# Performance work log

Measured on AMD Instinct MI355X. Metric: run time of the kernel, lower is better.

The kernel has to match this reference:

```python
import jax, jax.numpy as jnp
import numpy as np

B, S, D = 2, 4096, 768
H, DH = 12, 64
W = 256          # one-sided window (attention_window=512 // 2)
G = 8            # number of global tokens (first G positions)
NEG = -1e9


def setup_inputs() -> dict:
    key = jax.random.key(0)
    ks = jax.random.split(key, 8)
    hidden_states = jax.random.normal(ks[0], (B, S, D), dtype=jnp.float32)
    attention_mask = jnp.ones((B, S), dtype=jnp.float32)
    sc = 0.02
    Wq = jax.random.normal(ks[1], (D, D), dtype=jnp.float32) * sc
    Wk = jax.random.normal(ks[2], (D, D), dtype=jnp.float32) * sc
    Wv = jax.random.normal(ks[3], (D, D), dtype=jnp.float32) * sc
    Wqg = jax.random.normal(ks[4], (D, D), dtype=jnp.float32) * sc
    Wkg = jax.random.normal(ks[5], (D, D), dtype=jnp.float32) * sc
    Wvg = jax.random.normal(ks[6], (D, D), dtype=jnp.float32) * sc
    return {"hidden_states": hidden_states, "attention_mask": attention_mask,
            "Wq": Wq, "Wk": Wk, "Wv": Wv, "Wqg": Wqg, "Wkg": Wkg, "Wvg": Wvg}


def _heads(x):  # [B,S,D] -> [B,H,S,DH]
    return x.reshape(B, S, H, DH).transpose(0, 2, 1, 3)


def longformer_attn(hidden_states, attention_mask, Wq, Wk, Wv, Wqg, Wkg, Wvg):
    scale = 1.0 / jnp.sqrt(jnp.float32(DH))
    q = _heads(hidden_states @ Wq) * scale   # [B,H,S,DH]
    k = _heads(hidden_states @ Wk)
    v = _heads(hidden_states @ Wv)

    n = S // W                                # number of query chunks
    kp = jnp.pad(k, ((0, 0), (0, 0), (W, W), (0, 0)))
    vp = jnp.pad(v, ((0, 0), (0, 0), (W, W), (0, 0)))
    # window indices into padded seq: chunk i covers keys [i*W - W, i*W + 2W)
    idx = jnp.arange(n)[:, None] * W + jnp.arange(3 * W)[None, :]   # [n,3W]
    k_win = kp[:, :, idx]                     # [B,H,n,3W,DH]
    v_win = vp[:, :, idx]
    qc = q.reshape(B, H, n, W, DH)

    scores = jnp.einsum('bhnqd,bhnkd->bhnqk', qc, k_win)  # [B,H,n,W,3W]

    # masks: band (|key-query|<=W), valid key position, not a global key,
    # and key attention_mask
    rel = jnp.arange(3 * W)[None, :] - jnp.arange(W)[:, None]   # [W,3W] = k - q
    band = (rel >= 0) & (rel <= 2 * W)
    key_pos = idx - W                                           # [n,3W] real positions
    valid = (key_pos >= 0) & (key_pos < S) & (key_pos >= G)
    struct_mask = band[None, :, :] & valid[:, None, :]          # [n,W,3W]
    amp = jnp.pad(attention_mask, ((0, 0), (W, W)))
    am_win = amp[:, idx] > 0.5                                  # [B,n,3W]
    full_mask = struct_mask[None] & am_win[:, :, None, :]       # [B,n,W,3W]
    scores = jnp.where(full_mask[:, None], scores, NEG)

    # every query also attends to the G global keys (regular key projection)
    gk = k[:, :, :G]                                            # [B,H,G,DH]
    gscore = jnp.einsum('bhsd,bhgd->bhsg', q, gk).reshape(B, H, n, W, G)
    all_scores = jnp.concatenate([gscore, scores], axis=-1)     # [B,H,n,W,G+3W]
    probs = jax.nn.softmax(all_scores, axis=-1)

    gv = v[:, :, :G]
    out = (jnp.einsum('bhnqk,bhnkd->bhnqd', probs[..., G:], v_win)
           + jnp.einsum('bhnqg,bhgd->bhnqd', probs[..., :G], gv))
    out = out.reshape(B, H, S, DH)

    # global queries attend to ALL tokens with the *_global projections
    qg = _heads(hidden_states @ Wqg)[:, :, :G] * scale          # [B,H,G,DH]
    kg = _heads(hidden_states @ Wkg)
    vg = _heads(hidden_states @ Wvg)
    gs = jnp.einsum('bhgd,bhsd->bhgs', qg, kg)                  # [B,H,G,S]
    gs = jnp.where(attention_mask[:, None, None, :] > 0.5, gs, NEG)
    gp = jax.nn.softmax(gs, axis=-1)
    gout = jnp.einsum('bhgs,bhsd->bhgd', gp, vg)
    out = out.at[:, :, :G].set(gout)

    return out.transpose(0, 2, 1, 3).reshape(B, S, D)


def reference(hidden_states, attention_mask, Wq, Wk, Wv, Wqg, Wkg, Wvg):
    return longformer_attn(hidden_states, attention_mask, Wq, Wk, Wv, Wqg, Wkg, Wvg)
```

## Files before the change

kernel.cpp:

```cpp
#include <hip/hip_runtime.h>

#define B_ 2
#define S_ 4096
#define D_ 768
#define H_ 12
#define DH_ 64
#define W_ 256
#define G_ 8
#define NEG_ (-1e9f)
#define NC_ 64
#define CK_ 64
#define WQB 128
#define NT_ 11
#define NWIN (B_ * H_ * (S_ / WQB))

typedef __attribute__((ext_vector_type(4))) float f32x4;
typedef __attribute__((ext_vector_type(16))) float f32x16;
typedef __attribute__((ext_vector_type(8))) short s16x8;
typedef __attribute__((ext_vector_type(4))) short s16x4;
typedef unsigned short ushort_t;

__device__ __forceinline__ unsigned short f2bf(float f) {
    union { float f; unsigned u; } v; v.f = f;
    unsigned r = v.u + 0x7FFFu + ((v.u >> 16) & 1u);
    return (unsigned short)(r >> 16);
}
__device__ __forceinline__ float bf2f(unsigned short b) {
    union { unsigned u; float f; } v; v.u = ((unsigned)b) << 16;
    return v.f;
}
__device__ __forceinline__ unsigned cvtpk_bf16(float lo, float hi) {
    unsigned r;
    asm("v_cvt_pk_bf16_f32 %0, %1, %2" : "=v"(r) : "v"(lo), "v"(hi));
    return r;
}
__device__ __forceinline__ void gload16(const ushort_t* g, ushort_t* l) {
    __builtin_amdgcn_global_load_lds(
        (const __attribute__((address_space(1))) unsigned*)g,
        (__attribute__((address_space(3))) unsigned*)l, 16, 0, 0);
}
__device__ __forceinline__ float vmax16f(f32x16 v) {
    float a0 = fmaxf(v[0], v[1]), a1 = fmaxf(v[2], v[3]);
    float a2 = fmaxf(v[4], v[5]), a3 = fmaxf(v[6], v[7]);
    float a4 = fmaxf(v[8], v[9]), a5 = fmaxf(v[10], v[11]);
    float a6 = fmaxf(v[12], v[13]), a7 = fmaxf(v[14], v[15]);
    return fmaxf(fmaxf(fmaxf(a0, a1), fmaxf(a2, a3)),
                 fmaxf(fmaxf(a4, a5), fmaxf(a6, a7)));
}
__device__ __forceinline__ float vsum16f(f32x16 v) {
    float a0 = v[0] + v[1], a1 = v[2] + v[3];
    float a2 = v[4] + v[5], a3 = v[6] + v[7];
    float a4 = v[8] + v[9], a5 = v[10] + v[11];
    float a6 = v[12] + v[13], a7 = v[14] + v[15];
    return ((a0 + a1) + (a2 + a3)) + ((a4 + a5) + (a6 + a7));
}

__global__ __launch_bounds__(256) void fused_pre(const float* __restrict__ hs,
                                                 const float* __restrict__ W0,
                                                 const float* __restrict__ W1,
                                                 const float* __restrict__ W2,
                                                 const float* __restrict__ W3,
                                                 const float* __restrict__ W4,
                                                 const float* __restrict__ Wqg,
                                                 ushort_t* __restrict__ hs_bf,
                                                 ushort_t* __restrict__ wt,
                                                 float* __restrict__ qg) {
    __shared__ float smf[2 * D_];
    const int bid = blockIdx.x;
    const int t = threadIdx.x;

    if (bid < 3072) {
        const int i = bid * 256 + t;
        float4 a = *(const float4*)&hs[(size_t)i * 8];
        float4 c = *(const float4*)&hs[(size_t)i * 8 + 4];
        s16x8 o;
        o[0] = (short)f2bf(a.x); o[1] = (short)f2bf(a.y);
        o[2] = (short)f2bf(a.z); o[3] = (short)f2bf(a.w);
        o[4] = (short)f2bf(c.x); o[5] = (short)f2bf(c.y);
        o[6] = (short)f2bf(c.z); o[7] = (short)f2bf(c.w);
        *(s16x8*)&hs_bf[(size_t)i * 8] = o;
    } else if (bid < 5952) {
        const int bid2 = bid - 3072;
        const int w = bid2 / 576;
        const int rem = bid2 - w * 576;
        const int k0 = (rem / 24) * 32;
        const int n0 = (rem % 24) * 32;
        const float* Wsrc = (w == 0) ? W0 : (w == 1) ? W1 : (w == 2) ? W2 : (w == 3) ? W3 : W4;
        const float scl = (w == 0) ? 0.125f * 1.44269504f : 1.0f;
        const int r = t >> 3, c4 = (t & 7) * 4;
        float4 src = *(const float4*)&Wsrc[(size_t)(k0 + r) * D_ + n0 + c4];
        smf[r * 33 + c4 + 0] = src.x; smf[r * 33 + c4 + 1] = src.y;
        smf[r * 33 + c4 + 2] = src.z; smf[r * 33 + c4 + 3] = src.w;
        __syncthreads();
        s16x4 o;
        o[0] = (short)f2bf(smf[(c4 + 0) * 33 + r] * scl);
        o[1] = (short)f2bf(smf[(c4 + 1) * 33 + r] * scl);
        o[2] = (short)f2bf(smf[(c4 + 2) * 33 + r] * scl);
        o[3] = (short)f2bf(smf[(c4 + 3) * 33 + r] * scl);
        *(s16x4*)&wt[((size_t)(w * D_ + n0 + r)) * D_ + k0 + c4] = o;
    } else {
        const int bid3 = bid - 5952;
        const int rp = bid3 / 6;
        const int c0 = (bid3 - rp * 6) * 128;
        const int r = t >> 7, cl = t & 127;
        for (int i = t; i < 2 * D_; i += 256) {
            const int rr = i / D_, kk = i - rr * D_;
            const int row = rp * 2 + rr;
            const int b = row >> 3, g = row & 7;
            smf[rr * D_ + kk] = hs[((size_t)b * S_ + g) * D_ + kk];
        }
        __syncthreads();
        float a0 = 0.f, a1 = 0.f, a2 = 0.f, a3 = 0.f;
        const float* wp = &Wqg[c0 + cl];
        for (int kk = 0; kk < D_; kk += 4) {
            a0 += smf[r * D_ + kk + 0] * wp[(size_t)(kk + 0) * D_];
            a1 += smf[r * D_ + kk + 1] * wp[(size_t)(kk + 1) * D_];
            a2 += smf[r * D_ + kk + 2] * wp[(size_t)(kk + 2) * D_];
            a3 += smf[r * D_ + kk + 3] * wp[(size_t)(kk + 3) * D_];
        }
        const int row = rp * 2 + r;
        qg[(size_t)row * D_ + c0 + cl] = (a0 + a1 + a2 + a3) * 0.125f;
    }
}

__global__ __launch_bounds__(256, 2) void proj_mfma(const ushort_t* __restrict__ A,
                                                    const ushort_t* __restrict__ Bt,
                                                    ushort_t* __restrict__ oq,
                                                    ushort_t* __restrict__ ok,
                                                    ushort_t* __restrict__ ov,
                                                    ushort_t* __restrict__ okg,
                                                    ushort_t* __restrict__ ovg) {
    __shared__ char smem[34048];
    ushort_t* Al = (ushort_t*)smem;
    ushort_t* Bl = Al + 128 * 64;

    const int t = threadIdx.x;
    const int m0 = blockIdx.x * 128;
    const int n0 = blockIdx.y * 128;
    const int lane = t & 63;
    const int w = t >> 6;
    const int wm = (w >> 1) * 64, wn = (w & 1) * 64;
    const int ln = lane & 15, hi = lane >> 4;

    const int srow_in_call = lane >> 3;
    const int scol = ((lane & 7) ^ srow_in_call) * 8;

    f32x4 acc[4][4];
#pragma unroll
    for (int mi = 0; mi < 4; ++mi)
#pragma unroll
        for (int ni = 0; ni < 4; ++ni) acc[mi][ni] = (f32x4){0.f, 0.f, 0.f, 0.f};

    for (int k0 = 0; k0 < D_; k0 += 64) {
        __syncthreads();
#pragma unroll
        for (int j = 0; j < 4; ++j) {
            const int rbase = (w * 4 + j) * 8;
            const int row = rbase + srow_in_call;
            gload16(&A[(size_t)(m0 + row) * D_ + k0 + scol], &Al[rbase * 64]);
            gload16(&Bt[(size_t)(n0 + row) * D_ + k0 + scol], &Bl[rbase * 64]);
        }
        __syncthreads();

#pragma unroll
        for (int ks = 0; ks < 2; ++ks) {
            s16x8 af[4], bf[4];
#pragma unroll
            for (int i = 0; i < 4; ++i) {
                const int ar = wm + i * 16 + ln;
                const int br = wn + i * 16 + ln;
                const int slot = (4 * ks + hi) ^ (ln & 7);
                af[i] = *(const s16x8*)&Al[ar * 64 + slot * 8];
                bf[i] = *(const s16x8*)&Bl[br * 64 + slot * 8];
            }
#pragma unroll
            for (int mi = 0; mi < 4; ++mi)
#pragma unroll
                for (int ni = 0; ni < 4; ++ni)
                    acc[mi][ni] = __builtin_amdgcn_mfma_f32_16x16x32_bf16(af[mi], bf[ni], acc[mi][ni], 0, 0, 0);
        }
    }

    float* scr = (float*)smem;
    const int rl = t >> 2, cs = (t & 3) * 32;
    const int ng = n0 + cs;
    const int w_idx = ng / D_;
    const int cb = ng - w_idx * D_;
    const int hh = cb >> 6, dd = cb & 63;
    ushort_t* dst = (w_idx == 0) ? oq : (w_idx == 1) ? ok : (w_idx == 2) ? ov
                    : (w_idx == 3) ? okg : ovg;

#pragma unroll
    for (int r = 0; r < 2; ++r) {
        __syncthreads();
        if ((w >> 1) == r) {
#pragma unroll
            for (int mi = 0; mi < 4; ++mi)
#pragma unroll
                for (int ni = 0; ni < 4; ++ni)
#pragma unroll
                    for (int rr = 0; rr < 4; ++rr)
                        scr[(mi * 16 + hi * 4 + rr) * 132 + wn + ni * 16 + ln] = acc[mi][ni][rr];
        }
        __syncthreads();
        const int m = m0 + r * 64 + rl;
        const int bb = m >> 12, s = m & 4095;
        ushort_t* drow = dst + ((size_t)(bb * H_ + hh) * S_ + s) * DH_ + dd;
        const float* srcp = scr + rl * 132 + cs;
#pragma unroll
        for (int seg = 0; seg < 4; ++seg) {
            float4 lo = *(const float4*)&srcp[seg * 8];
            float4 hi4 = *(const float4*)&srcp[seg * 8 + 4];
            s16x8 o;
            o[0] = (short)f2bf(lo.x); o[1] = (short)f2bf(lo.y);
            o[2] = (short)f2bf(lo.z); o[3] = (short)f2bf(lo.w);
            o[4] = (short)f2bf(hi4.x); o[5] = (short)f2bf(hi4.y);
            o[6] = (short)f2bf(hi4.z); o[7] = (short)f2bf(hi4.w);
            *(s16x8*)&drow[seg * 8] = o;
        }
    }
}

__global__ __launch_bounds__(256, 2) void win_glob(const ushort_t* __restrict__ q,
                                                   const ushort_t* __restrict__ k,
                                                   const ushort_t* __restrict__ v,
                                                   const float* __restrict__ am,
                                                   float* __restrict__ out,
                                                   const float* __restrict__ qg,
                                                   const ushort_t* __restrict__ kg,
                                                   const ushort_t* __restrict__ vg,
                                                   float* __restrict__ pout,
                                                   float* __restrict__ pm,
                                                   float* __restrict__ pl) {
    __shared__ char smem[39424];
    const int bid = blockIdx.x;
    const int t = threadIdx.x;

    if (bid >= NWIN) {
        const int idx = bid - NWIN;
        const int c = idx & 63;
        const int hb = idx >> 6;
        const int h = hb % H_;
        const int b = hb / H_;
        const int bh = b * H_ + h;
        const size_t base = (size_t)bh * S_ * DH_;
        const int jg0 = c * CK_;

        float* qs = (float*)smem;
        float* kt = qs + G_ * DH_;
        float* vt = kt + CK_ * 69;
        float* ps = vt + CK_ * 68;

        for (int i = t; i < G_ * DH_; i += 256)
            qs[(i >> 6) * DH_ + (i & 63)] = qg[(size_t)(b * G_ + (i >> 6)) * D_ + h * DH_ + (i & 63)];
        {
            const int row = t >> 2, off = (t & 3) * 16;
            const ushort_t* kr = &kg[base + (size_t)(jg0 + row) * DH_ + off];
            const ushort_t* vr = &vg[base + (size_t)(jg0 + row) * DH_ + off];
            s16x8 ka = *(const s16x8*)kr;
            s16x8 kb2 = *(const s16x8*)(kr + 8);
            s16x8 va = *(const s16x8*)vr;
            s16x8 vb = *(const s16x8*)(vr + 8);
#pragma unroll
            for (int i = 0; i < 8; ++i) {
                kt[row * 69 + off + i] = bf2f((ushort_t)ka[i]);
                kt[row * 69 + off + 8 + i] = bf2f((ushort_t)kb2[i]);
                vt[row * 68 + off + i] = bf2f((ushort_t)va[i]);
                vt[row * 68 + off + 8 + i] = bf2f((ushort_t)vb[i]);
            }
        }
        __syncthreads();

        const int g = t >> 5, jl = t & 31;
        float sc0 = 0.f, sc1 = 0.f;
#pragma unroll 8
        for (int d = 0; d < DH_; ++d) {
            const float qv = qs[g * DH_ + d];
            sc0 += qv * kt[jl * 69 + d];
            sc1 += qv * kt[(jl + 32) * 69 + d];
        }
        if (!(am[(size_t)b * S_ + jg0 + jl] > 0.5f)) sc0 = NEG_;
        if (!(am[(size_t)b * S_ + jg0 + jl + 32] > 0.5f)) sc1 = NEG_;

        float mm = fmaxf(sc0, sc1);
        mm = fmaxf(mm, __shfl_xor(mm, 1));
        mm = fmaxf(mm, __shfl_xor(mm, 2));
        mm = fmaxf(mm, __shfl_xor(mm, 4));
        mm = fmaxf(mm, __shfl_xor(mm, 8));
        mm = fmaxf(mm, __shfl_xor(mm, 16));
        const float p0 = __expf(sc0 - mm);
        const float p1 = __expf(sc1 - mm);
        float ls = p0 + p1;
        ls += __shfl_xor(ls, 1);
        ls += __shfl_xor(ls, 2);
        ls += __shfl_xor(ls, 4);
        ls += __shfl_xor(ls, 8);
        ls += __shfl_xor(ls, 16);
        ps[g * CK_ + jl] = p0;
        ps[g * CK_ + jl + 32] = p1;
        if (jl == 0) {
            pm[((size_t)bh * NC_ + c) * G_ + g] = mm;
            pl[((size_t)bh * NC_ + c) * G_ + g] = ls;
        }
        __syncthreads();

#pragma unroll
        for (int pass = 0; pass < 2; ++pass) {
            const int gg = (t >> 6) + pass * 4;
            const int d = t & 63;
            float acc = 0.f;
#pragma unroll 8
            for (int j = 0; j < CK_; ++j) acc += ps[gg * CK_ + j] * vt[j * 68 + d];
            pout[(((size_t)bh * NC_ + c) * G_ + gg) * DH_ + d] = acc;
        }
        return;
    }

    ushort_t* Kl = (ushort_t*)smem;
    ushort_t* Vt = Kl + 64 * 72;
    unsigned* Mv = (unsigned*)(Vt + 64 * 66);
    float* Ow = (float*)smem;

    const int wg = (bid & 7) * 96 + (bid >> 3);
    const int n = wg & 31;
    const int h = (wg >> 5) % H_;
    const int b = wg / (32 * H_);

    const int lane = t & 63, w = t >> 6;
    const int l31 = lane & 31, h5 = lane >> 5;
    const int q0w = n * WQB + w * 32;
    const int q_abs = q0w + l31;
    const size_t bh = (size_t)(b * H_ + h) * S_;

    s16x8 qf[4];
#pragma unroll
    for (int ks = 0; ks < 4; ++ks)
        qf[ks] = *(const s16x8*)&q[(bh + q_abs) * DH_ + ks * 16 + 8 * h5];

    f32x16 oacc[2];
#pragma unroll
    for (int dt = 0; dt < 2; ++dt)
#pragma unroll
        for (int i = 0; i < 16; ++i) oacc[dt][i] = 0.f;
    float m_run, l_run;

    const int srow = t >> 2, soff = (t & 3) * 16;

    {
        const ushort_t* krow = &k[(bh + srow) * DH_ + soff];
        s16x8 k0v = *(const s16x8*)krow;
        s16x8 k1v = *(const s16x8*)(krow + 8);
        *(s16x8*)&Kl[srow * 72 + soff] = k0v;
        *(s16x8*)&Kl[srow * 72 + soff + 8] = k1v;
        const ushort_t* vrow = &v[(bh + srow) * DH_ + soff];
        s16x8 v0v = *(const s16x8*)vrow;
        s16x8 v1v = *(const s16x8*)(vrow + 8);
#pragma unroll
        for (int i = 0; i < 8; ++i) {
            Vt[(soff + i) * 66 + srow] = (ushort_t)v0v[i];
            Vt[(soff + 8 + i) * 66 + srow] = (ushort_t)v1v[i];
        }
    }
    __syncthreads();

    {
        f32x16 s0;
#pragma unroll
        for (int i = 0; i < 16; ++i) s0[i] = 0.f;
#pragma unroll
        for (int ks = 0; ks < 4; ++ks) {
            s16x8 kf = *(const s16x8*)&Kl[l31 * 72 + ks * 16 + 8 * h5];
            s0 = __builtin_amdgcn_mfma_f32_32x32x16_bf16(kf, qf[ks], s0, 0, 0, 0);
        }
        float tmax = fmaxf(fmaxf(s0[0], s0[1]), fmaxf(s0[2], s0[3]));
        tmax = fmaxf(tmax, __shfl_xor(tmax, 32));
        m_run = tmax;
        float p0 = exp2f(s0[0] - m_run), p1 = exp2f(s0[1] - m_run);
        float p2 = exp2f(s0[2] - m_run), p3 = exp2f(s0[3] - m_run);
        float psum = (p0 + p1) + (p2 + p3);
        psum += __shfl_xor(psum, 32);
        l_run = psum;
        const unsigned Au = cvtpk_bf16(p0, p1);
        const unsigned Bu = cvtpk_bf16(p2, p3);
        const unsigned send0 = h5 ? Au : 0u;
        const unsigned send1 = h5 ? Bu : 0u;
        const unsigned recv0 = __shfl_xor((int)send0, 32);
        const unsigned recv1 = __shfl_xor((int)send1, 32);
        union { unsigned u[4]; s16x8 v8; } pu;
        pu.u[0] = h5 ? recv0 : Au;
        pu.u[1] = h5 ? recv1 : Bu;
        pu.u[2] = h5 ? 0u : recv0;
        pu.u[3] = h5 ? 0u : recv1;
#pragma unroll
        for (int dt = 0; dt < 2; ++dt) {
            const int vbase = (dt * 32 + l31) * 66 + 8 * h5;
            union { unsigned u[4]; s16x8 v8; } vf;
            vf.u[0] = *(const unsigned*)&Vt[vbase + 0];
            vf.u[1] = *(const unsigned*)&Vt[vbase + 2];
            vf.u[2] = *(const unsigned*)&Vt[vbase + 4];
            vf.u[3] = *(const unsigned*)&Vt[vbase + 6];
            oacc[dt] = __builtin_amdgcn_mfma_f32_32x32x16_bf16(vf.v8, pu.v8, oacc[dt], 0, 0, 0);
        }
    }

    for (int tt = 1; tt < NT_; ++tt) {
        const int pbase = n * WQB - W_ + (tt - 1) * 64;
        __syncthreads();
        {
            const int p = pbase + srow;
            const int pr = p < 0 ? 0 : (p >= S_ ? S_ - 1 : p);
            const ushort_t* krow = &k[(bh + pr) * DH_ + soff];
            s16x8 k0v = *(const s16x8*)krow;
            s16x8 k1v = *(const s16x8*)(krow + 8);
            *(s16x8*)&Kl[srow * 72 + soff] = k0v;
            *(s16x8*)&Kl[srow * 72 + soff + 8] = k1v;
            const ushort_t* vrow = &v[(bh + pr) * DH_ + soff];
            s16x8 v0v = *(const s16x8*)vrow;
            s16x8 v1v = *(const s16x8*)(vrow + 8);
#pragma unroll
            for (int i = 0; i < 8; ++i) {
                Vt[(soff + i) * 66 + srow] = (ushort_t)v0v[i];
                Vt[(soff + 8 + i) * 66 + srow] = (ushort_t)v1v[i];
            }
        }
        if (w == 0) {
            const int p2 = pbase + lane;
            const bool ok = (p2 >= G_) && (p2 < S_) &&
                            (am[(size_t)b * S_ + (p2 < 0 ? 0 : (p2 >= S_ ? S_ - 1 : p2))] > 0.5f);
            unsigned long long bal = __ballot(ok);
            if (lane == 0) { Mv[0] = (unsigned)bal; Mv[1] = (unsigned)(bal >> 32); }
        }
        __syncthreads();

        if (pbase > q0w + 31 + W_ || pbase + 63 < q0w - W_) continue;

        f32x16 sc[2];
#pragma unroll
        for (int st = 0; st < 2; ++st)
#pragma unroll
            for (int i = 0; i < 16; ++i) sc[st][i] = 0.f;
#pragma unroll
        for (int st = 0; st < 2; ++st)
#pragma unroll
            for (int ks = 0; ks < 4; ++ks) {
                s16x8 kf = *(const s16x8*)&Kl[(st * 32 + l31) * 72 + ks * 16 + 8 * h5];
                sc[st] = __builtin_amdgcn_mfma_f32_32x32x16_bf16(kf, qf[ks], sc[st], 0, 0, 0);
            }

        const unsigned mv0 = Mv[0], mv1 = Mv[1];
        const bool fullt = ((mv0 & mv1) == 0xFFFFFFFFu) &&
                           (pbase >= q0w + 31 - W_) && (pbase + 63 <= q0w + W_);
        if (!fullt) {
#pragma unroll
            for (int st = 0; st < 2; ++st)
#pragma unroll
                for (int reg = 0; reg < 16; ++reg) {
                    const int cst = (reg & 3) + 8 * (reg >> 2);
                    const int crow = cst + 4 * h5;
                    const int key_abs = pbase + st * 32 + crow;
                    const unsigned mvx = (st == 0) ? mv0 : mv1;
                    const bool valid = ((mvx >> crow) & 1u) &&
                                       (key_abs >= q_abs - W_) && (key_abs <= q_abs + W_);
                    sc[st][reg] = valid ? sc[st][reg] : -1e30f;
                }
        }
        float tmax = fmaxf(vmax16f(sc[0]), vmax16f(sc[1]));
        tmax = fmaxf(tmax, __shfl_xor(tmax, 32));

        if (__any(tmax > m_run + 11.5f)) {
            const float mnew = fmaxf(m_run, tmax);
            const float f = exp2f(m_run - mnew);
            l_run *= f;
#pragma unroll
            for (int dt = 0; dt < 2; ++dt)
#pragma unroll
                for (int i = 0; i < 16; ++i) oacc[dt][i] *= f;
            m_run = mnew;
        }
#pragma unroll
        for (int st = 0; st < 2; ++st)
#pragma unroll
            for (int reg = 0; reg < 16; ++reg)
                sc[st][reg] = exp2f(sc[st][reg] - m_run);
        float psum = vsum16f(sc[0]) + vsum16f(sc[1]);
        psum += __shfl_xor(psum, 32);
        l_run += psum;

#pragma unroll
        for (int ks = 0; ks < 4; ++ks) {
            const int st = ks >> 1, k8 = (ks & 1) * 8;
            const unsigned Au = cvtpk_bf16(sc[st][k8 + 0], sc[st][k8 + 1]);
            const unsigned Bu = cvtpk_bf16(sc[st][k8 + 2], sc[st][k8 + 3]);
            const unsigned Cu = cvtpk_bf16(sc[st][k8 + 4], sc[st][k8 + 5]);
            const unsigned Du = cvtpk_bf16(sc[st][k8 + 6], sc[st][k8 + 7]);
            const unsigned send0 = h5 ? Au : Cu;
            const unsigned send1 = h5 ? Bu : Du;
            const unsigned recv0 = __shfl_xor((int)send0, 32);
            const unsigned recv1 = __shfl_xor((int)send1, 32);
            union { unsigned u[4]; s16x8 v8; } pu;
            pu.u[0] = h5 ? recv0 : Au;
            pu.u[1] = h5 ? recv1 : Bu;
            pu.u[2] = h5 ? Cu : recv0;
            pu.u[3] = h5 ? Du : recv1;
#pragma unroll
            for (int dt = 0; dt < 2; ++dt) {
                const int vbase = (dt * 32 + l31) * 66 + ks * 16 + 8 * h5;
                union { unsigned u[4]; s16x8 v8; } vf;
                vf.u[0] = *(const unsigned*)&Vt[vbase + 0];
                vf.u[1] = *(const unsigned*)&Vt[vbase + 2];
                vf.u[2] = *(const unsigned*)&Vt[vbase + 4];
                vf.u[3] = *(const unsigned*)&Vt[vbase + 6];
                oacc[dt] = __builtin_amdgcn_mfma_f32_32x32x16_bf16(vf.v8, pu.v8, oacc[dt], 0, 0, 0);
            }
        }
    }

    __syncthreads();
    const float inv = 1.0f / l_run;
    float* OwW = Ow + w * 32 * 68;
#pragma unroll
    for (int dt = 0; dt < 2; ++dt)
#pragma unroll
        for (int reg = 0; reg < 16; ++reg) {
            const int d = dt * 32 + (reg & 3) + 8 * (reg >> 2) + 4 * h5;
            OwW[l31 * 68 + d] = oacc[dt][reg] * inv;
        }
    asm volatile("s_waitcnt lgkmcnt(0)" ::: "memory");
    const int qq = lane >> 1, half = lane & 1;
    const float* src = &OwW[qq * 68 + half * 32];
    float* dstp = &out[((size_t)b * S_ + q0w + qq) * D_ + h * DH_ + half * 32];
#pragma unroll
    for (int j = 0; j < 8; ++j)
        *(float4*)&dstp[j * 4] = *(const float4*)&src[j * 4];
}

__global__ __launch_bounds__(256) void glob_reduce(const float* __restrict__ pout,
                                                   const float* __restrict__ pm,
                                                   const float* __restrict__ pl,
                                                   float* __restrict__ out) {
    const int bh = blockIdx.x;
    const int b = bh / H_, h = bh - b * H_;
    const int t = threadIdx.x;

    __shared__ float wc[G_][NC_];
    __shared__ float wsum[G_];

    const int g = t >> 5, cl = t & 31;
    const float m0 = pm[((size_t)bh * NC_ + cl) * G_ + g];
    const float m1 = pm[((size_t)bh * NC_ + cl + 32) * G_ + g];
    float M = fmaxf(m0, m1);
    M = fmaxf(M, __shfl_xor(M, 1));
    M = fmaxf(M, __shfl_xor(M, 2));
    M = fmaxf(M, __shfl_xor(M, 4));
    M = fmaxf(M, __shfl_xor(M, 8));
    M = fmaxf(M, __shfl_xor(M, 16));
    const float w0 = __expf(m0 - M);
    const float w1 = __expf(m1 - M);
    float S = w0 * pl[((size_t)bh * NC_ + cl) * G_ + g] +
              w1 * pl[((size_t)bh * NC_ + cl + 32) * G_ + g];
    S += __shfl_xor(S, 1);
    S += __shfl_xor(S, 2);
    S += __shfl_xor(S, 4);
    S += __shfl_xor(S, 8);
    S += __shfl_xor(S, 16);
    wc[g][cl] = w0;
    wc[g][cl + 32] = w1;
    if (cl == 0) wsum[g] = S;
    __syncthreads();

#pragma unroll
    for (int pass = 0; pass < 2; ++pass) {
        const int gg = (t >> 6) + pass * 4;
        const int d = t & 63;
        float acc = 0.f;
        for (int c2 = 0; c2 < NC_; ++c2)
            acc += wc[gg][c2] * pout[(((size_t)bh * NC_ + c2) * G_ + gg) * DH_ + d];
        out[((size_t)b * S_ + gg) * D_ + h * DH_ + d] = acc / wsum[gg];
    }
}

extern "C" void kernel_launch(void* const* d_in, const int* in_sizes, int n_in,
                              void* d_out, int out_size, void* d_ws, size_t ws_size,
                              hipStream_t stream) {
    (void)in_sizes; (void)n_in; (void)out_size; (void)ws_size;

    const float* hs    = (const float*)d_in[0];
    const float* amask = (const float*)d_in[1];
    const float* Wq    = (const float*)d_in[2];
    const float* Wk    = (const float*)d_in[3];
    const float* Wv    = (const float*)d_in[4];
    const float* Wqg   = (const float*)d_in[5];
    const float* Wkg   = (const float*)d_in[6];
    const float* Wvg   = (const float*)d_in[7];
    float* out = (float*)d_out;

    char* p = (char*)d_ws;
    ushort_t* hs_bf = (ushort_t*)p; p += (size_t)B_ * S_ * D_ * 2;
    ushort_t* wt    = (ushort_t*)p; p += (size_t)5 * D_ * D_ * 2;
    const size_t per = (size_t)B_ * H_ * S_ * DH_;
    ushort_t* qb  = (ushort_t*)p; p += per * 2;
    ushort_t* kb  = (ushort_t*)p; p += per * 2;
    ushort_t* vb  = (ushort_t*)p; p += per * 2;
    ushort_t* kgb = (ushort_t*)p; p += per * 2;
    ushort_t* vgb = (ushort_t*)p; p += per * 2;
    float* qg   = (float*)p; p += (size_t)B_ * G_ * D_ * 4;
    float* pout = (float*)p; p += (size_t)B_ * H_ * NC_ * G_ * DH_ * 4;
    float* pm   = (float*)p; p += (size_t)B_ * H_ * NC_ * G_ * 4;
    float* pl   = (float*)p;

    fused_pre<<<6000, 256, 0, stream>>>(hs, Wq, Wk, Wv, Wkg, Wvg, Wqg, hs_bf, wt, qg);
    proj_mfma<<<dim3(B_ * S_ / 128, 5 * D_ / 128), 256, 0, stream>>>(hs_bf, wt, qb, kb, vb, kgb, vgb);
    win_glob<<<NWIN + NC_ * H_ * B_, 256, 0, stream>>>(qb, kb, vb, amask, out,
                                                       qg, kgb, vgb, pout, pm, pl);
    glob_reduce<<<B_ * H_, 256, 0, stream>>>(pout, pm, pl, out);
}
```

Measured before the change: 142.0 us.

## Prefetch next K/V tile into registers and precompute key masks upfront

Software-pipelines the windowed attention loop: the next 64-key K/V tile is loaded from global memory into registers while the current tile is computed, then written to LDS at the top of the next iteration. The per-tile attention-mask ballots are all computed once before the loop into a larger Mv array, which removes the per-iteration mask work from the critical path. This adds register pressure, and Mv must be large enough for 20 entries; if Mv was declared with only two entries, the writes would overflow.

```diff
diff --git a/kernel.cpp b/kernel.cpp
--- a/kernel.cpp
+++ b/kernel.cpp
@@ -361,7 +361,32 @@
             Vt[(soff + 8 + i) * 66 + srow] = (ushort_t)v1v[i];
         }
     }
+    if (w == 0) {
+#pragma unroll
+        for (int tt = 1; tt < NT_; ++tt) {
+            const int p2 = n * WQB - W_ + (tt - 1) * 64 + lane;
+            const bool ok = (p2 >= G_) && (p2 < S_) &&
+                            (am[(size_t)b * S_ + (p2 < 0 ? 0 : (p2 >= S_ ? S_ - 1 : p2))] > 0.5f);
+            unsigned long long bal = __ballot(ok);
+            if (lane == 0) {
+                Mv[2 * (tt - 1)] = (unsigned)bal;
+                Mv[2 * (tt - 1) + 1] = (unsigned)(bal >> 32);
+            }
+        }
+    }
     __syncthreads();
+
+    s16x8 kr0, kr1, vr0, vr1;
+    {
+        const int p = n * WQB - W_ + srow;
+        const int pr = p < 0 ? 0 : p;
+        const ushort_t* krow = &k[(bh + pr) * DH_ + soff];
+        kr0 = *(const s16x8*)krow;
+        kr1 = *(const s16x8*)(krow + 8);
+        const ushort_t* vrow = &v[(bh + pr) * DH_ + soff];
+        vr0 = *(const s16x8*)vrow;
+        vr1 = *(const s16x8*)(vrow + 8);
+    }
 
     {
         f32x16 s0;
@@ -406,31 +431,25 @@
     for (int tt = 1; tt < NT_; ++tt) {
         const int pbase = n * WQB - W_ + (tt - 1) * 64;
         __syncthreads();
-        {
-            const int p = pbase + srow;
+        *(s16x8*)&Kl[srow * 72 + soff] = kr0;
+        *(s16x8*)&Kl[srow * 72 + soff + 8] = kr1;
+#pragma unroll
+        for (int i = 0; i < 8; ++i) {
+            Vt[(soff + i) * 66 + srow] = (ushort_t)vr0[i];
+            Vt[(soff + 8 + i) * 66 + srow] = (ushort_t)vr1[i];
+        }
+        __syncthreads();
+
+        if (tt < NT_ - 1) {
+            const int p = pbase + 64 + srow;
             const int pr = p < 0 ? 0 : (p >= S_ ? S_ - 1 : p);
             const ushort_t* krow = &k[(bh + pr) * DH_ + soff];
-            s16x8 k0v = *(const s16x8*)krow;
-            s16x8 k1v = *(const s16x8*)(krow + 8);
-            *(s16x8*)&Kl[srow * 72 + soff] = k0v;
-            *(s16x8*)&Kl[srow * 72 + soff + 8] = k1v;
+            kr0 = *(const s16x8*)krow;
+            kr1 = *(const s16x8*)(krow + 8);
             const ushort_t* vrow = &v[(bh + pr) * DH_ + soff];
-            s16x8 v0v = *(const s16x8*)vrow;
-            s16x8 v1v = *(const s16x8*)(vrow + 8);
-#pragma unroll
-            for (int i = 0; i < 8; ++i) {
-                Vt[(soff + i) * 66 + srow] = (ushort_t)v0v[i];
-                Vt[(soff + 8 + i) * 66 + srow] = (ushort_t)v1v[i];
-            }
-        }
-        if (w == 0) {
-            const int p2 = pbase + lane;
-            const bool ok = (p2 >= G_) && (p2 < S_) &&
-                            (am[(size_t)b * S_ + (p2 < 0 ? 0 : (p2 >= S_ ? S_ - 1 : p2))] > 0.5f);
-            unsigned long long bal = __ballot(ok);
-            if (lane == 0) { Mv[0] = (unsigned)bal; Mv[1] = (unsigned)(bal >> 32); }
-        }
-        __syncthreads();
+            vr0 = *(const s16x8*)vrow;
+            vr1 = *(const s16x8*)(vrow + 8);
+        }
 
         if (pbase > q0w + 31 + W_ || pbase + 63 < q0w - W_) continue;
 
@@ -447,7 +466,7 @@
                 sc[st] = __builtin_amdgcn_mfma_f32_32x32x16_bf16(kf, qf[ks], sc[st], 0, 0, 0);
             }
 
-        const unsigned mv0 = Mv[0], mv1 = Mv[1];
+        const unsigned mv0 = Mv[2 * (tt - 1)], mv1 = Mv[2 * (tt - 1) + 1];
         const bool fullt = ((mv0 & mv1) == 0xFFFFFFFFu) &&
                            (pbase >= q0w + 31 - W_) && (pbase + 63 <= q0w + W_);
         if (!fullt) {
```

After: 151.4 us. 6.6% more time.

## Shrink win_glob shared memory with bf16 tiles and two-phase output staging

Applied to the files above, without the earlier changes.

The global-token branch now keeps K and V tiles in shared memory as raw bf16 instead of converting them to fp32, and unpacks the values on the fly in the dot-product loops. The window branch's epilogue stages its output through shared memory in two halves, two waves at a time, so it needs only half the staging buffer. Together these cut the static shared allocation from about 39 KB to about 22 KB, aiming to fit more blocks per CU. The cost is an extra barrier in the epilogue and extra bit-unpacking ALU work in the global branch.

```diff
diff --git a/kernel.cpp b/kernel.cpp
--- a/kernel.cpp
+++ b/kernel.cpp
@@ -27,6 +27,10 @@
 }
 __device__ __forceinline__ float bf2f(unsigned short b) {
     union { unsigned u; float f; } v; v.u = ((unsigned)b) << 16;
+    return v.f;
+}
+__device__ __forceinline__ float bfbits(unsigned u) {
+    union { unsigned u; float f; } v; v.u = u;
     return v.f;
 }
 __device__ __forceinline__ unsigned cvtpk_bf16(float lo, float hi) {
@@ -232,7 +236,7 @@
                                                    float* __restrict__ pout,
                                                    float* __restrict__ pm,
                                                    float* __restrict__ pl) {
-    __shared__ char smem[39424];
+    __shared__ __align__(16) char smem[22016];
     const int bid = blockIdx.x;
     const int t = threadIdx.x;
 
@@ -247,9 +251,9 @@
         const int jg0 = c * CK_;
 
         float* qs = (float*)smem;
-        float* kt = qs + G_ * DH_;
-        float* vt = kt + CK_ * 69;
-        float* ps = vt + CK_ * 68;
+        ushort_t* kt = (ushort_t*)(smem + 2048);
+        ushort_t* vt = (ushort_t*)(smem + 2048 + 9472);
+        float* ps = (float*)(smem + 2048 + 9472 + 8448);
 
         for (int i = t; i < G_ * DH_; i += 256)
             qs[(i >> 6) * DH_ + (i & 63)] = qg[(size_t)(b * G_ + (i >> 6)) * D_ + h * DH_ + (i & 63)];
@@ -257,16 +261,19 @@
             const int row = t >> 2, off = (t & 3) * 16;
             const ushort_t* kr = &kg[base + (size_t)(jg0 + row) * DH_ + off];
             const ushort_t* vr = &vg[base + (size_t)(jg0 + row) * DH_ + off];
-            s16x8 ka = *(const s16x8*)kr;
-            s16x8 kb2 = *(const s16x8*)(kr + 8);
-            s16x8 va = *(const s16x8*)vr;
-            s16x8 vb = *(const s16x8*)(vr + 8);
-#pragma unroll
-            for (int i = 0; i < 8; ++i) {
-                kt[row * 69 + off + i] = bf2f((ushort_t)ka[i]);
-                kt[row * 69 + off + 8 + i] = bf2f((ushort_t)kb2[i]);
-                vt[row * 68 + off + i] = bf2f((ushort_t)va[i]);
-                vt[row * 68 + off + 8 + i] = bf2f((ushort_t)vb[i]);
+            union { s16x8 v8; unsigned u[4]; } a0, a1, b0, b1;
+            a0.v8 = *(const s16x8*)kr;
+            a1.v8 = *(const s16x8*)(kr + 8);
+            b0.v8 = *(const s16x8*)vr;
+            b1.v8 = *(const s16x8*)(vr + 8);
+            unsigned* kd = (unsigned*)&kt[row * 74 + off];
+            unsigned* vd = (unsigned*)&vt[row * 66 + off];
+#pragma unroll
+            for (int i = 0; i < 4; ++i) {
+                kd[i] = a0.u[i];
+                kd[4 + i] = a1.u[i];
+                vd[i] = b0.u[i];
+                vd[4 + i] = b1.u[i];
             }
         }
         __syncthreads();
@@ -274,10 +281,13 @@
         const int g = t >> 5, jl = t & 31;
         float sc0 = 0.f, sc1 = 0.f;
 #pragma unroll 8
-        for (int d = 0; d < DH_; ++d) {
-            const float qv = qs[g * DH_ + d];
-            sc0 += qv * kt[jl * 69 + d];
-            sc1 += qv * kt[(jl + 32) * 69 + d];
+        for (int d = 0; d < DH_; d += 2) {
+            const unsigned k0p = *(const unsigned*)&kt[jl * 74 + d];
+            const unsigned k1p = *(const unsigned*)&kt[(jl + 32) * 74 + d];
+            const float q0v = qs[g * DH_ + d];
+            const float q1v = qs[g * DH_ + d + 1];
+            sc0 += q0v * bfbits(k0p << 16) + q1v * bfbits(k0p & 0xFFFF0000u);
+            sc1 += q0v * bfbits(k1p << 16) + q1v * bfbits(k1p & 0xFFFF0000u);
         }
         if (!(am[(size_t)b * S_ + jg0 + jl] > 0.5f)) sc0 = NEG_;
         if (!(am[(size_t)b * S_ + jg0 + jl + 32] > 0.5f)) sc1 = NEG_;
@@ -310,7 +320,7 @@
             const int d = t & 63;
             float acc = 0.f;
 #pragma unroll 8
-            for (int j = 0; j < CK_; ++j) acc += ps[gg * CK_ + j] * vt[j * 68 + d];
+            for (int j = 0; j < CK_; ++j) acc += ps[gg * CK_ + j] * bf2f(vt[j * 66 + d]);
             pout[(((size_t)bh * NC_ + c) * G_ + gg) * DH_ + d] = acc;
         }
         return;
@@ -515,23 +525,43 @@
         }
     }
 
+    const float inv = 1.0f / l_run;
     __syncthreads();
-    const float inv = 1.0f / l_run;
-    float* OwW = Ow + w * 32 * 68;
-#pragma unroll
-    for (int dt = 0; dt < 2; ++dt)
-#pragma unroll
-        for (int reg = 0; reg < 16; ++reg) {
-            const int d = dt * 32 + (reg & 3) + 8 * (reg >> 2) + 4 * h5;
-            OwW[l31 * 68 + d] = oacc[dt][reg] * inv;
-        }
-    asm volatile("s_waitcnt lgkmcnt(0)" ::: "memory");
-    const int qq = lane >> 1, half = lane & 1;
-    const float* src = &OwW[qq * 68 + half * 32];
-    float* dstp = &out[((size_t)b * S_ + q0w + qq) * D_ + h * DH_ + half * 32];
-#pragma unroll
-    for (int j = 0; j < 8; ++j)
-        *(float4*)&dstp[j * 4] = *(const float4*)&src[j * 4];
+    if (w < 2) {
+        float* OwW = Ow + (w & 1) * 32 * 68;
+#pragma unroll
+        for (int dt = 0; dt < 2; ++dt)
+#pragma unroll
+            for (int reg = 0; reg < 16; ++reg) {
+                const int d = dt * 32 + (reg & 3) + 8 * (reg >> 2) + 4 * h5;
+                OwW[l31 * 68 + d] = oacc[dt][reg] * inv;
+            }
+        asm volatile("s_waitcnt lgkmcnt(0)" ::: "memory");
+        const int qq = lane >> 1, half = lane & 1;
+        const float* src = &OwW[qq * 68 + half * 32];
+        float* dstp = &out[((size_t)b * S_ + q0w + qq) * D_ + h * DH_ + half * 32];
+#pragma unroll
+        for (int j = 0; j < 8; ++j)
+            *(float4*)&dstp[j * 4] = *(const float4*)&src[j * 4];
+    }
+    __syncthreads();
+    if (w >= 2) {
+        float* OwW = Ow + (w & 1) * 32 * 68;
+#pragma unroll
+        for (int dt = 0; dt < 2; ++dt)
+#pragma unroll
+            for (int reg = 0; reg < 16; ++reg) {
+                const int d = dt * 32 + (reg & 3) + 8 * (reg >> 2) + 4 * h5;
+                OwW[l31 * 68 + d] = oacc[dt][reg] * inv;
+            }
+        asm volatile("s_waitcnt lgkmcnt(0)" ::: "memory");
+        const int qq = lane >> 1, half = lane & 1;
+        const float* src = &OwW[qq * 68 + half * 32];
+        float* dstp = &out[((size_t)b * S_ + q0w + qq) * D_ + h * DH_ + half * 32];
+#pragma unroll
+        for (int j = 0; j < 8; ++j)
+            *(float4*)&dstp[j * 4] = *(const float4*)&src[j * 4];
+    }
 }
 
 __global__ __launch_bounds__(256) void glob_reduce(const float* __restrict__ pout,
```

Result: no change. 140.3 us, median of 2 (-1.2%).
